# Performance work log

Hardware: AMD Instinct MI355X
Metric: run time of the kernel (lower is better)

The kernel has to match this reference:

```python
import jax, jax.numpy as jnp
import numpy as np


def setup_inputs() -> dict:
    key = jax.random.key(0)
    k_x, k_wxh, k_whh, k_fcw, k_fcb = jax.random.split(key, 5)
    B, T, I, H = 256, 512, 64, 512
    x = jax.random.normal(k_x, (B, T, I), dtype=jnp.float32)
    W_xh = jax.random.normal(k_wxh, (I, H), dtype=jnp.float32) * 0.01
    W_hh = jax.random.normal(k_whh, (H, H), dtype=jnp.float32) * 0.01
    b = jnp.zeros((H,), dtype=jnp.float32)
    # nn.Linear(H, 1): weight (1, H), bias (1); init ~ U(-1/sqrt(H), 1/sqrt(H))
    lim = 1.0 / np.sqrt(H)
    fc_w = jax.random.uniform(k_fcw, (1, H), dtype=jnp.float32, minval=-lim, maxval=lim)
    fc_b = jax.random.uniform(k_fcb, (1,), dtype=jnp.float32, minval=-lim, maxval=lim)
    return {"x": x, "W_xh": W_xh, "W_hh": W_hh, "b": b, "fc_w": fc_w, "fc_b": fc_b}


def reference(x, W_xh, W_hh, b, fc_w, fc_b):
    B, T, I = x.shape
    H = W_hh.shape[0]
    # Precompute input projections for all timesteps in one big matmul: (B,T,H)
    xh = jnp.einsum('bti,ih->bth', x, W_xh) + b
    h0 = jnp.zeros((B, H), dtype=x.dtype)

    def step(h, xh_t):
        h_new = jnp.tanh(xh_t + h @ W_hh)
        return h_new, None

    h_final, _ = jax.lax.scan(step, h0, jnp.swapaxes(xh, 0, 1))  # scan over T
    return h_final @ fc_w.T + fc_b  # (B, 1)
```

## Files before the change

### kernel.cpp

```cpp
#include <hip/hip_runtime.h>


#define BATCH    256
#define TSTEPS   512
#define IDIM     64
#define HDIM     512
#define NTH      512

typedef _Float16 half2_t __attribute__((ext_vector_type(2)));
typedef _Float16 half8_t __attribute__((ext_vector_type(8)));

union H8U {
    half8_t v;
    half2_t p[4];
    uint4   u4;
};

__device__ __forceinline__ float fdot2(half2_t a, half2_t b, float c) {
#if __has_builtin(__builtin_amdgcn_fdot2)
    return __builtin_amdgcn_fdot2(a, b, c, false);
#else
    return c + (float)a[0] * (float)b[0] + (float)a[1] * (float)b[1];
#endif
}

__device__ __forceinline__ float fast_tanh(float x) {
    float e = __builtin_amdgcn_exp2f(x * 2.88539008177792681472f);
    return 1.0f - 2.0f * __builtin_amdgcn_rcpf(e + 1.0f);
}

#define XH_ROWS 16
__global__ __launch_bounds__(NTH, 4)
void xh_gemm(const float* __restrict__ x, const float* __restrict__ Wxh,
             const float* __restrict__ bias, _Float16* __restrict__ xh)
{
    const int j = threadIdx.x;
    const size_t r0 = (size_t)blockIdx.x * XH_ROWS;
    float wcol[IDIM];
#pragma unroll
    for (int i = 0; i < IDIM; ++i) wcol[i] = Wxh[(size_t)i * HDIM + j];
    const float bj = bias[j];
#pragma unroll
    for (int r = 0; r < XH_ROWS; ++r) {
        const float* xr = x + (r0 + r) * IDIM;
        float acc = bj;
#pragma unroll
        for (int i = 0; i < IDIM; ++i) acc += xr[i] * wcol[i];
        xh[(r0 + r) * HDIM + j] = (_Float16)acc;
    }
}

#define S_RP   208
#define S_RC   52
#define S_LC   12
#define S_LSTR 13
#define S_LDSW_BYTES (512 * S_LSTR * 16)
#define S_HBUF_OFF   S_LDSW_BYTES
#define S_HBUF_ELEMS 512
#define S_RED_OFF    (S_HBUF_OFF + 2 * S_HBUF_ELEMS * 2)
#define S_SMEM_BYTES (S_RED_OFF + 64)

__global__ __attribute__((amdgpu_flat_work_group_size(NTH, NTH), amdgpu_waves_per_eu(2, 2)))
void rnn_split(const _Float16* __restrict__ xh,
               const float* __restrict__ Whh,
               const float* __restrict__ fcw,
               const float* __restrict__ fcb,
               float* __restrict__ out)
{
    extern __shared__ char smem[];
    uint4*    ldsW = reinterpret_cast<uint4*>(smem);
    _Float16* hbuf = reinterpret_cast<_Float16*>(smem + S_HBUF_OFF);
    float*    red  = reinterpret_cast<float*>(smem + S_RED_OFF);

    const int j = threadIdx.x;
    const int b = blockIdx.x;

    half2_t wreg[S_RP];
#pragma unroll
    for (int p = 0; p < S_RP; ++p) {
        const int k = 2 * p;
        half2_t w;
        w[0] = (_Float16)Whh[(size_t)k * HDIM + j];
        w[1] = (_Float16)Whh[(size_t)(k + 1) * HDIM + j];
        wreg[p] = w;
    }
#pragma unroll
    for (int cc = 0; cc < S_LC; ++cc) {
        H8U u;
#pragma unroll
        for (int q = 0; q < 4; ++q) {
            const int k0 = 416 + 8 * cc + 2 * q;
            half2_t w;
            w[0] = (_Float16)Whh[(size_t)k0 * HDIM + j];
            w[1] = (_Float16)Whh[(size_t)(k0 + 1) * HDIM + j];
            u.p[q] = w;
        }
        ldsW[j * S_LSTR + cc] = u.u4;
    }

    const float fcwj = fcw[j];
    const _Float16* xhb = xh + (size_t)b * TSTEPS * HDIM;

    hbuf[j] = (_Float16)0.0f;
    __syncthreads();

    float hval = 0.0f;
    for (int t = 0; t < TSTEPS; ++t) {
        const int cur = t & 1;
        const int nxt = cur ^ 1;
        const _Float16* hb = hbuf + cur * S_HBUF_ELEMS;

        const float xv = (float)xhb[(size_t)t * HDIM + j];

        float a0 = 0.0f, a1 = 0.0f, a2 = 0.0f, a3 = 0.0f;
#pragma unroll
        for (int c = 0; c < S_RC; ++c) {
            H8U u;
            u.v = *reinterpret_cast<const half8_t*>(hb + 8 * c);
            a0 = fdot2(u.p[0], wreg[4 * c + 0], a0);
            a1 = fdot2(u.p[1], wreg[4 * c + 1], a1);
            a2 = fdot2(u.p[2], wreg[4 * c + 2], a2);
            a3 = fdot2(u.p[3], wreg[4 * c + 3], a3);
        }
#pragma unroll
        for (int cc = 0; cc < S_LC; ++cc) {
            H8U u, w;
            u.v  = *reinterpret_cast<const half8_t*>(hb + 8 * (S_RC + cc));
            w.u4 = ldsW[j * S_LSTR + cc];
            a0 = fdot2(u.p[0], w.p[0], a0);
            a1 = fdot2(u.p[1], w.p[1], a1);
            a2 = fdot2(u.p[2], w.p[2], a2);
            a3 = fdot2(u.p[3], w.p[3], a3);
        }
        hval = fast_tanh(((a0 + a1) + (a2 + a3)) + xv);

        hbuf[nxt * S_HBUF_ELEMS + j] = (_Float16)hval;
        __syncthreads();
    }

    float partial = hval * fcwj;
#pragma unroll
    for (int off = 32; off >= 1; off >>= 1)
        partial += __shfl_down(partial, off, 64);
    if ((j & 63) == 0) red[j >> 6] = partial;
    __syncthreads();
    if (j == 0) {
        float s = 0.0f;
#pragma unroll
        for (int w = 0; w < 8; ++w) s += red[w];
        out[b] = s + fcb[0];
    }
}

#define F_RP   216
#define F_RC   54
#define F_LC   18
#define F_LSTR 19
#define F_LDSW_BYTES (512 * F_LSTR * 16)
#define F_HBUF_OFF   F_LDSW_BYTES
#define F_HBUF_ELEMS 640
#define F_RED_OFF    (F_HBUF_OFF + 2 * F_HBUF_ELEMS * 2)
#define F_SMEM_BYTES (F_RED_OFF + 64)

__global__ __attribute__((amdgpu_flat_work_group_size(NTH, NTH), amdgpu_waves_per_eu(2, 2)))
void rnn_fused(const float* __restrict__ x, const float* __restrict__ Wxh,
               const float* __restrict__ Whh, const float* __restrict__ bias,
               const float* __restrict__ fcw, const float* __restrict__ fcb,
               float* __restrict__ out)
{
    extern __shared__ char smem[];
    uint4*    ldsW = reinterpret_cast<uint4*>(smem);
    _Float16* hbuf = reinterpret_cast<_Float16*>(smem + F_HBUF_OFF);
    float*    red  = reinterpret_cast<float*>(smem + F_RED_OFF);

    const int j = threadIdx.x;
    const int b = blockIdx.x;

    half2_t wreg[F_RP];
#pragma unroll
    for (int p = 0; p < F_RP; ++p) {
        const int k = 2 * p;
        half2_t w;
        w[0] = (_Float16)Whh[(size_t)k * HDIM + j];
        w[1] = (_Float16)Whh[(size_t)(k + 1) * HDIM + j];
        wreg[p] = w;
    }
#pragma unroll
    for (int cc = 0; cc < F_LC; ++cc) {
        H8U u;
#pragma unroll
        for (int q = 0; q < 4; ++q) {
            const int k0 = 432 + 8 * cc + 2 * q;
            const int k1 = k0 + 1;
            half2_t w;
            w[0] = (_Float16)(k0 < HDIM ? Whh[(size_t)k0 * HDIM + j]
                                        : Wxh[(size_t)(k0 - HDIM) * HDIM + j]);
            w[1] = (_Float16)(k1 < HDIM ? Whh[(size_t)k1 * HDIM + j]
                                        : Wxh[(size_t)(k1 - HDIM) * HDIM + j]);
            u.p[q] = w;
        }
        ldsW[j * F_LSTR + cc] = u.u4;
    }

    const float bj   = bias[j];
    const float fcwj = fcw[j];

    hbuf[j] = (_Float16)0.0f;
    if (j < IDIM) hbuf[HDIM + j] = (_Float16)x[((size_t)b * TSTEPS + 0) * IDIM + j];
    __syncthreads();

    float hval = 0.0f;
    for (int t = 0; t < TSTEPS; ++t) {
        const int cur = t & 1;
        const int nxt = cur ^ 1;
        const _Float16* hb = hbuf + cur * F_HBUF_ELEMS;

        float xv = 0.0f;
        const bool do_x = (j < IDIM) && (t + 1 < TSTEPS);
        if (do_x) xv = x[((size_t)b * TSTEPS + (t + 1)) * IDIM + j];

        float a0 = bj, a1 = 0.0f, a2 = 0.0f, a3 = 0.0f;
#pragma unroll
        for (int c = 0; c < F_RC; ++c) {
            H8U u;
            u.v = *reinterpret_cast<const half8_t*>(hb + 8 * c);
            a0 = fdot2(u.p[0], wreg[4 * c + 0], a0);
            a1 = fdot2(u.p[1], wreg[4 * c + 1], a1);
            a2 = fdot2(u.p[2], wreg[4 * c + 2], a2);
            a3 = fdot2(u.p[3], wreg[4 * c + 3], a3);
        }
#pragma unroll
        for (int cc = 0; cc < F_LC; ++cc) {
            H8U u, w;
            u.v  = *reinterpret_cast<const half8_t*>(hb + 8 * (F_RC + cc));
            w.u4 = ldsW[j * F_LSTR + cc];
            a0 = fdot2(u.p[0], w.p[0], a0);
            a1 = fdot2(u.p[1], w.p[1], a1);
            a2 = fdot2(u.p[2], w.p[2], a2);
            a3 = fdot2(u.p[3], w.p[3], a3);
        }
        hval = fast_tanh((a0 + a1) + (a2 + a3));

        hbuf[nxt * F_HBUF_ELEMS + j] = (_Float16)hval;
        if (do_x) hbuf[nxt * F_HBUF_ELEMS + HDIM + j] = (_Float16)xv;
        __syncthreads();
    }

    float partial = hval * fcwj;
#pragma unroll
    for (int off = 32; off >= 1; off >>= 1)
        partial += __shfl_down(partial, off, 64);
    if ((j & 63) == 0) red[j >> 6] = partial;
    __syncthreads();
    if (j == 0) {
        float s = 0.0f;
#pragma unroll
        for (int w = 0; w < 8; ++w) s += red[w];
        out[b] = s + fcb[0];
    }
}

extern "C" void kernel_launch(void* const* d_in, const int* in_sizes, int n_in,
                              void* d_out, int out_size, void* d_ws, size_t ws_size,
                              hipStream_t stream) {
    const float* x    = (const float*)d_in[0];
    const float* Wxh  = (const float*)d_in[1];
    const float* Whh  = (const float*)d_in[2];
    const float* bias = (const float*)d_in[3];
    const float* fcw  = (const float*)d_in[4];
    const float* fcb  = (const float*)d_in[5];
    float* out = (float*)d_out;

    const size_t xh_bytes = (size_t)BATCH * TSTEPS * HDIM * sizeof(_Float16);
    if (ws_size >= xh_bytes) {
        hipFuncSetAttribute(reinterpret_cast<const void*>(rnn_split),
                            hipFuncAttributeMaxDynamicSharedMemorySize, S_SMEM_BYTES);
        _Float16* xh = (_Float16*)d_ws;
        xh_gemm<<<(BATCH * TSTEPS) / XH_ROWS, NTH, 0, stream>>>(x, Wxh, bias, xh);
        rnn_split<<<BATCH, NTH, S_SMEM_BYTES, stream>>>(xh, Whh, fcw, fcb, out);
    } else {
        hipFuncSetAttribute(reinterpret_cast<const void*>(rnn_fused),
                            hipFuncAttributeMaxDynamicSharedMemorySize, F_SMEM_BYTES);
        rnn_fused<<<BATCH, NTH, F_SMEM_BYTES, stream>>>(x, Wxh, Whh, bias, fcw, fcb, out);
    }
}
```

Baseline: 1.144 ms.

## Split recurrent matvec across thread quads with DPP reduction, 1024 threads per block

Replaces the one-thread-per-hidden-unit recurrence kernel with a 1024-thread version. Each group of four threads covers two hidden units, each thread handles a quarter of the K dimension, and the partial sums are combined with DPP quad reductions. This shortens each thread's serial dot-product chain per timestep and spreads the W_hh fp16 cache over more registers. The h buffer layout is padded to reduce LDS bank conflicts. In exchange it adds cross-lane reduction latency and leaves three of every four lanes idle during the tanh and store.

```diff
diff --git a/kernel.cpp b/kernel.cpp
--- a/kernel.cpp
+++ b/kernel.cpp
@@ -27,6 +27,16 @@
 __device__ __forceinline__ float fast_tanh(float x) {
     float e = __builtin_amdgcn_exp2f(x * 2.88539008177792681472f);
     return 1.0f - 2.0f * __builtin_amdgcn_rcpf(e + 1.0f);
+}
+
+__device__ __forceinline__ float quad_sum(float x) {
+    union { float f; int i; } a, b;
+    a.f = x;
+    b.i = __builtin_amdgcn_update_dpp(0, a.i, 0xB1, 0xF, 0xF, true);
+    a.f += b.f;
+    b.i = __builtin_amdgcn_update_dpp(0, a.i, 0x4E, 0xF, 0xF, true);
+    a.f += b.f;
+    return a.f;
 }
 
 #define XH_ROWS 16
@@ -50,104 +60,139 @@
     }
 }
 
-#define S_RP   208
-#define S_RC   52
-#define S_LC   12
-#define S_LSTR 13
-#define S_LDSW_BYTES (512 * S_LSTR * 16)
-#define S_HBUF_OFF   S_LDSW_BYTES
-#define S_HBUF_ELEMS 512
-#define S_RED_OFF    (S_HBUF_OFF + 2 * S_HBUF_ELEMS * 2)
-#define S_SMEM_BYTES (S_RED_OFF + 64)
-
-__global__ __attribute__((amdgpu_flat_work_group_size(NTH, NTH), amdgpu_waves_per_eu(2, 2)))
-void rnn_split(const _Float16* __restrict__ xh,
-               const float* __restrict__ Whh,
-               const float* __restrict__ fcw,
-               const float* __restrict__ fcb,
-               float* __restrict__ out)
+#define NTH2      1024
+#define Q_CHUNKS  16
+#define Q_AREG    12
+#define Q_BREG    11
+#define Q_LCH     9
+#define Q_LDSW_BYTES (NTH2 * Q_LCH * 16)
+#define Q_HB_OFF     Q_LDSW_BYTES
+#define Q_HB_STRIDE  1152
+#define Q_RED_OFF    (Q_HB_OFF + 2 * Q_HB_STRIDE)
+#define Q_SMEM_BYTES (Q_RED_OFF + 64)
+
+__global__ __attribute__((amdgpu_flat_work_group_size(NTH2, NTH2)))
+void rnn_quad(const _Float16* __restrict__ xh,
+              const float* __restrict__ Whh,
+              const float* __restrict__ fcw,
+              const float* __restrict__ fcb,
+              float* __restrict__ out)
 {
     extern __shared__ char smem[];
-    uint4*    ldsW = reinterpret_cast<uint4*>(smem);
-    _Float16* hbuf = reinterpret_cast<_Float16*>(smem + S_HBUF_OFF);
-    float*    red  = reinterpret_cast<float*>(smem + S_RED_OFF);
-
-    const int j = threadIdx.x;
-    const int b = blockIdx.x;
-
-    half2_t wreg[S_RP];
-#pragma unroll
-    for (int p = 0; p < S_RP; ++p) {
-        const int k = 2 * p;
-        half2_t w;
-        w[0] = (_Float16)Whh[(size_t)k * HDIM + j];
-        w[1] = (_Float16)Whh[(size_t)(k + 1) * HDIM + j];
-        wreg[p] = w;
-    }
-#pragma unroll
-    for (int cc = 0; cc < S_LC; ++cc) {
-        H8U u;
-#pragma unroll
-        for (int q = 0; q < 4; ++q) {
-            const int k0 = 416 + 8 * cc + 2 * q;
-            half2_t w;
-            w[0] = (_Float16)Whh[(size_t)k0 * HDIM + j];
-            w[1] = (_Float16)Whh[(size_t)(k0 + 1) * HDIM + j];
-            u.p[q] = w;
-        }
-        ldsW[j * S_LSTR + cc] = u.u4;
-    }
-
-    const float fcwj = fcw[j];
-    const _Float16* xhb = xh + (size_t)b * TSTEPS * HDIM;
-
-    hbuf[j] = (_Float16)0.0f;
+    uint4* ldsW = reinterpret_cast<uint4*>(smem);
+    float* red  = reinterpret_cast<float*>(smem + Q_RED_OFF);
+
+    const int tid = threadIdx.x;
+    const int q   = tid & 3;
+    const int co  = (tid >> 2) & 15;
+    const int wv  = tid >> 6;
+    const int jA  = wv * 32 + co * 2;
+    const int b   = blockIdx.x;
+
+    half2_t wAr[4 * Q_AREG];
+    half2_t wBr[4 * Q_BREG];
+    uint4*  myW = ldsW + tid * Q_LCH;
+#pragma unroll
+    for (int i = 0; i < Q_CHUNKS; ++i) {
+        H8U a, c;
+#pragma unroll
+        for (int e = 0; e < 4; ++e) {
+            const int k = 128 * q + 8 * i + 2 * e;
+            const float2 r0 = *reinterpret_cast<const float2*>(Whh + (size_t)k * HDIM + jA);
+            const float2 r1 = *reinterpret_cast<const float2*>(Whh + (size_t)(k + 1) * HDIM + jA);
+            half2_t ha; ha[0] = (_Float16)r0.x; ha[1] = (_Float16)r1.x;
+            half2_t hc; hc[0] = (_Float16)r0.y; hc[1] = (_Float16)r1.y;
+            if (i < Q_AREG) wAr[4 * i + e] = ha; else a.p[e] = ha;
+            if (i < Q_BREG) wBr[4 * i + e] = hc; else c.p[e] = hc;
+        }
+        if (i >= Q_AREG) myW[i - Q_AREG]       = a.u4;
+        if (i >= Q_BREG) myW[4 + (i - Q_BREG)] = c.u4;
+    }
+
+    const _Float16* hb0 = reinterpret_cast<const _Float16*>(smem + Q_HB_OFF + 288 * q);
+    const _Float16* hb1 = reinterpret_cast<const _Float16*>(smem + Q_HB_OFF + Q_HB_STRIDE + 288 * q);
+    _Float16* wp0 = reinterpret_cast<_Float16*>(smem + Q_HB_OFF + 2 * jA + 32 * (jA >> 7));
+    _Float16* wp1 = reinterpret_cast<_Float16*>(smem + Q_HB_OFF + Q_HB_STRIDE + 2 * jA + 32 * (jA >> 7));
+
+    const float fcwA = fcw[jA];
+    const float fcwB = fcw[jA + 1];
+    const _Float16* xhp = xh + (size_t)b * TSTEPS * HDIM + jA;
+
+    if (q == 0) {
+        half2_t z; z[0] = (_Float16)0.f; z[1] = (_Float16)0.f;
+        *reinterpret_cast<half2_t*>(wp0) = z;
+    }
     __syncthreads();
 
-    float hval = 0.0f;
+    float hA = 0.f, hB = 0.f;
+#pragma unroll 1
     for (int t = 0; t < TSTEPS; ++t) {
-        const int cur = t & 1;
-        const int nxt = cur ^ 1;
-        const _Float16* hb = hbuf + cur * S_HBUF_ELEMS;
-
-        const float xv = (float)xhb[(size_t)t * HDIM + j];
-
-        float a0 = 0.0f, a1 = 0.0f, a2 = 0.0f, a3 = 0.0f;
-#pragma unroll
-        for (int c = 0; c < S_RC; ++c) {
-            H8U u;
-            u.v = *reinterpret_cast<const half8_t*>(hb + 8 * c);
-            a0 = fdot2(u.p[0], wreg[4 * c + 0], a0);
-            a1 = fdot2(u.p[1], wreg[4 * c + 1], a1);
-            a2 = fdot2(u.p[2], wreg[4 * c + 2], a2);
-            a3 = fdot2(u.p[3], wreg[4 * c + 3], a3);
-        }
-#pragma unroll
-        for (int cc = 0; cc < S_LC; ++cc) {
-            H8U u, w;
-            u.v  = *reinterpret_cast<const half8_t*>(hb + 8 * (S_RC + cc));
-            w.u4 = ldsW[j * S_LSTR + cc];
-            a0 = fdot2(u.p[0], w.p[0], a0);
-            a1 = fdot2(u.p[1], w.p[1], a1);
-            a2 = fdot2(u.p[2], w.p[2], a2);
-            a3 = fdot2(u.p[3], w.p[3], a3);
-        }
-        hval = fast_tanh(((a0 + a1) + (a2 + a3)) + xv);
-
-        hbuf[nxt * S_HBUF_ELEMS + j] = (_Float16)hval;
+        const _Float16* hb = (t & 1) ? hb1 : hb0;
+        const half2_t xv = *reinterpret_cast<const half2_t*>(xhp);
+        xhp += HDIM;
+
+        float a0 = 0.f, a1 = 0.f, c0 = 0.f, c1 = 0.f;
+#pragma unroll
+        for (int i = 0; i < Q_BREG; ++i) {
+            H8U u; u.v = *reinterpret_cast<const half8_t*>(hb + 8 * i);
+            a0 = fdot2(u.p[0], wAr[4*i+0], a0);
+            a1 = fdot2(u.p[1], wAr[4*i+1], a1);
+            a0 = fdot2(u.p[2], wAr[4*i+2], a0);
+            a1 = fdot2(u.p[3], wAr[4*i+3], a1);
+            c0 = fdot2(u.p[0], wBr[4*i+0], c0);
+            c1 = fdot2(u.p[1], wBr[4*i+1], c1);
+            c0 = fdot2(u.p[2], wBr[4*i+2], c0);
+            c1 = fdot2(u.p[3], wBr[4*i+3], c1);
+        }
+        {
+            H8U u; u.v = *reinterpret_cast<const half8_t*>(hb + 8 * 11);
+            H8U wc; wc.u4 = myW[4];
+            a0 = fdot2(u.p[0], wAr[44], a0);
+            a1 = fdot2(u.p[1], wAr[45], a1);
+            a0 = fdot2(u.p[2], wAr[46], a0);
+            a1 = fdot2(u.p[3], wAr[47], a1);
+            c0 = fdot2(u.p[0], wc.p[0], c0);
+            c1 = fdot2(u.p[1], wc.p[1], c1);
+            c0 = fdot2(u.p[2], wc.p[2], c0);
+            c1 = fdot2(u.p[3], wc.p[3], c1);
+        }
+#pragma unroll
+        for (int i = 12; i < 16; ++i) {
+            H8U u; u.v = *reinterpret_cast<const half8_t*>(hb + 8 * i);
+            H8U wa; wa.u4 = myW[i - 12];
+            H8U wc; wc.u4 = myW[i - 7];
+            a0 = fdot2(u.p[0], wa.p[0], a0);
+            a1 = fdot2(u.p[1], wa.p[1], a1);
+            a0 = fdot2(u.p[2], wa.p[2], a0);
+            a1 = fdot2(u.p[3], wa.p[3], a1);
+            c0 = fdot2(u.p[0], wc.p[0], c0);
+            c1 = fdot2(u.p[1], wc.p[1], c1);
+            c0 = fdot2(u.p[2], wc.p[2], c0);
+            c1 = fdot2(u.p[3], wc.p[3], c1);
+        }
+
+        const float sA = quad_sum(a0 + a1);
+        const float sB = quad_sum(c0 + c1);
+
+        if (q == 0) {
+            hA = fast_tanh(sA + (float)xv[0]);
+            hB = fast_tanh(sB + (float)xv[1]);
+            half2_t hw; hw[0] = (_Float16)hA; hw[1] = (_Float16)hB;
+            *reinterpret_cast<half2_t*>((t & 1) ? wp0 : wp1) = hw;
+        }
         __syncthreads();
     }
 
-    float partial = hval * fcwj;
+    float partial = (q == 0) ? (hA * fcwA + hB * fcwB) : 0.f;
 #pragma unroll
     for (int off = 32; off >= 1; off >>= 1)
         partial += __shfl_down(partial, off, 64);
-    if ((j & 63) == 0) red[j >> 6] = partial;
+    if ((tid & 63) == 0) red[tid >> 6] = partial;
     __syncthreads();
-    if (j == 0) {
-        float s = 0.0f;
-#pragma unroll
-        for (int w = 0; w < 8; ++w) s += red[w];
+    if (tid == 0) {
+        float s = 0.f;
+#pragma unroll
+        for (int w = 0; w < 16; ++w) s += red[w];
         out[b] = s + fcb[0];
     }
 }
@@ -189,15 +234,15 @@
     for (int cc = 0; cc < F_LC; ++cc) {
         H8U u;
 #pragma unroll
-        for (int q = 0; q < 4; ++q) {
-            const int k0 = 432 + 8 * cc + 2 * q;
+        for (int qq = 0; qq < 4; ++qq) {
+            const int k0 = 432 + 8 * cc + 2 * qq;
             const int k1 = k0 + 1;
             half2_t w;
             w[0] = (_Float16)(k0 < HDIM ? Whh[(size_t)k0 * HDIM + j]
                                         : Wxh[(size_t)(k0 - HDIM) * HDIM + j]);
             w[1] = (_Float16)(k1 < HDIM ? Whh[(size_t)k1 * HDIM + j]
                                         : Wxh[(size_t)(k1 - HDIM) * HDIM + j]);
-            u.p[q] = w;
+            u.p[qq] = w;
         }
         ldsW[j * F_LSTR + cc] = u.u4;
     }
@@ -273,11 +318,11 @@
 
     const size_t xh_bytes = (size_t)BATCH * TSTEPS * HDIM * sizeof(_Float16);
     if (ws_size >= xh_bytes) {
-        hipFuncSetAttribute(reinterpret_cast<const void*>(rnn_split),
-                            hipFuncAttributeMaxDynamicSharedMemorySize, S_SMEM_BYTES);
+        hipFuncSetAttribute(reinterpret_cast<const void*>(rnn_quad),
+                            hipFuncAttributeMaxDynamicSharedMemorySize, Q_SMEM_BYTES);
         _Float16* xh = (_Float16*)d_ws;
         xh_gemm<<<(BATCH * TSTEPS) / XH_ROWS, NTH, 0, stream>>>(x, Wxh, bias, xh);
-        rnn_split<<<BATCH, NTH, S_SMEM_BYTES, stream>>>(xh, Whh, fcw, fcb, out);
+        rnn_quad<<<BATCH, NTH2, Q_SMEM_BYTES, stream>>>(xh, Whh, fcw, fcb, out);
     } else {
         hipFuncSetAttribute(reinterpret_cast<const void*>(rnn_fused),
                             hipFuncAttributeMaxDynamicSharedMemorySize, F_SMEM_BYTES);
```

Result: slower. 1.425 ms (+24.5%).

## Split RNN recurrence K-dimension across thread quads with DPP reduction

Applied to the files above, without the earlier changes.

The recurrent kernel now gives each thread four output columns over a 128-wide slice of K, instead of one column over the full K. Partial sums are combined across the four threads of a quad with DPP lane swizzles. The h buffer is padded per quarter so that each thread reads only its own slice. This cuts per-thread LDS reads of h by roughly 4x and reuses each loaded h vector across four columns. The cost is the cross-lane reduction and a new, more complex LDS addressing layout.

```diff
diff --git a/kernel.cpp b/kernel.cpp
--- a/kernel.cpp
+++ b/kernel.cpp
@@ -27,6 +27,16 @@
 __device__ __forceinline__ float fast_tanh(float x) {
     float e = __builtin_amdgcn_exp2f(x * 2.88539008177792681472f);
     return 1.0f - 2.0f * __builtin_amdgcn_rcpf(e + 1.0f);
+}
+
+__device__ __forceinline__ float quad_sum(float x) {
+    union { float f; int i; } a, b;
+    a.f = x;
+    b.i = __builtin_amdgcn_update_dpp(0, a.i, 0xB1, 0xF, 0xF, true);
+    a.f += b.f;
+    b.i = __builtin_amdgcn_update_dpp(0, a.i, 0x4E, 0xF, 0xF, true);
+    a.f += b.f;
+    return a.f;
 }
 
 #define XH_ROWS 16
@@ -50,102 +60,138 @@
     }
 }
 
-#define S_RP   208
-#define S_RC   52
-#define S_LC   12
-#define S_LSTR 13
-#define S_LDSW_BYTES (512 * S_LSTR * 16)
-#define S_HBUF_OFF   S_LDSW_BYTES
-#define S_HBUF_ELEMS 512
-#define S_RED_OFF    (S_HBUF_OFF + 2 * S_HBUF_ELEMS * 2)
-#define S_SMEM_BYTES (S_RED_OFF + 64)
+#define K4_RP      48
+#define K4_STR     17
+#define K4_W_BYTES (NTH * K4_STR * 16)
+#define K4_HB_OFF   K4_W_BYTES
+#define K4_HB_STRIDE 1152
+#define K4_RED_OFF  (K4_HB_OFF + 2 * K4_HB_STRIDE)
+#define K4_SMEM_BYTES (K4_RED_OFF + 64)
 
 __global__ __attribute__((amdgpu_flat_work_group_size(NTH, NTH), amdgpu_waves_per_eu(2, 2)))
-void rnn_split(const _Float16* __restrict__ xh,
-               const float* __restrict__ Whh,
-               const float* __restrict__ fcw,
-               const float* __restrict__ fcb,
-               float* __restrict__ out)
+void rnn_k4(const _Float16* __restrict__ xh,
+            const float* __restrict__ Whh,
+            const float* __restrict__ fcw,
+            const float* __restrict__ fcb,
+            float* __restrict__ out)
 {
     extern __shared__ char smem[];
-    uint4*    ldsW = reinterpret_cast<uint4*>(smem);
-    _Float16* hbuf = reinterpret_cast<_Float16*>(smem + S_HBUF_OFF);
-    float*    red  = reinterpret_cast<float*>(smem + S_RED_OFF);
-
-    const int j = threadIdx.x;
-    const int b = blockIdx.x;
-
-    half2_t wreg[S_RP];
-#pragma unroll
-    for (int p = 0; p < S_RP; ++p) {
-        const int k = 2 * p;
+    uint4* ldsW = reinterpret_cast<uint4*>(smem);
+    float* red  = reinterpret_cast<float*>(smem + K4_RED_OFF);
+
+    const int tid   = threadIdx.x;
+    const int q     = tid & 3;
+    const int c     = tid >> 2;
+    const int j0    = 4 * c;
+    const int kbase = 128 * q;
+    const int b     = blockIdx.x;
+
+    half2_t wr0[K4_RP], wr1[K4_RP], wr2[K4_RP], wr3[K4_RP];
+    uint4*  myW = ldsW + tid * K4_STR;
+#pragma unroll
+    for (int p = 0; p < K4_RP; ++p) {
+        const float4 f0 = *reinterpret_cast<const float4*>(Whh + (size_t)(kbase + 2 * p) * HDIM + j0);
+        const float4 f1 = *reinterpret_cast<const float4*>(Whh + (size_t)(kbase + 2 * p + 1) * HDIM + j0);
         half2_t w;
-        w[0] = (_Float16)Whh[(size_t)k * HDIM + j];
-        w[1] = (_Float16)Whh[(size_t)(k + 1) * HDIM + j];
-        wreg[p] = w;
-    }
-#pragma unroll
-    for (int cc = 0; cc < S_LC; ++cc) {
-        H8U u;
-#pragma unroll
-        for (int q = 0; q < 4; ++q) {
-            const int k0 = 416 + 8 * cc + 2 * q;
+        w[0] = (_Float16)f0.x; w[1] = (_Float16)f1.x; wr0[p] = w;
+        w[0] = (_Float16)f0.y; w[1] = (_Float16)f1.y; wr1[p] = w;
+        w[0] = (_Float16)f0.z; w[1] = (_Float16)f1.z; wr2[p] = w;
+        w[0] = (_Float16)f0.w; w[1] = (_Float16)f1.w; wr3[p] = w;
+    }
+#pragma unroll
+    for (int cc = 0; cc < 4; ++cc) {
+        H8U t0, t1, t2, t3;
+#pragma unroll
+        for (int e = 0; e < 4; ++e) {
+            const int k = kbase + 96 + 8 * cc + 2 * e;
+            const float4 f0 = *reinterpret_cast<const float4*>(Whh + (size_t)k * HDIM + j0);
+            const float4 f1 = *reinterpret_cast<const float4*>(Whh + (size_t)(k + 1) * HDIM + j0);
             half2_t w;
-            w[0] = (_Float16)Whh[(size_t)k0 * HDIM + j];
-            w[1] = (_Float16)Whh[(size_t)(k0 + 1) * HDIM + j];
-            u.p[q] = w;
-        }
-        ldsW[j * S_LSTR + cc] = u.u4;
-    }
-
-    const float fcwj = fcw[j];
-    const _Float16* xhb = xh + (size_t)b * TSTEPS * HDIM;
-
-    hbuf[j] = (_Float16)0.0f;
+            w[0] = (_Float16)f0.x; w[1] = (_Float16)f1.x; t0.p[e] = w;
+            w[0] = (_Float16)f0.y; w[1] = (_Float16)f1.y; t1.p[e] = w;
+            w[0] = (_Float16)f0.z; w[1] = (_Float16)f1.z; t2.p[e] = w;
+            w[0] = (_Float16)f0.w; w[1] = (_Float16)f1.w; t3.p[e] = w;
+        }
+        myW[cc]      = t0.u4;
+        myW[4 + cc]  = t1.u4;
+        myW[8 + cc]  = t2.u4;
+        myW[12 + cc] = t3.u4;
+    }
+
+    const char* hb0c = smem + K4_HB_OFF + 288 * q;
+    const char* hb1c = hb0c + K4_HB_STRIDE;
+    const int   jw   = j0 + q;
+    const int   wbyte = 2 * jw + 32 * (jw >> 7);
+    _Float16* wp0 = reinterpret_cast<_Float16*>(smem + K4_HB_OFF + wbyte);
+    _Float16* wp1 = reinterpret_cast<_Float16*>(smem + K4_HB_OFF + K4_HB_STRIDE + wbyte);
+
+    const float fcwj = fcw[jw];
+    const _Float16* xhp = xh + (size_t)b * TSTEPS * HDIM + jw;
+
+    if (tid < 144) {
+        uint4 z; z.x = z.y = z.z = z.w = 0u;
+        reinterpret_cast<uint4*>(smem + K4_HB_OFF)[tid] = z;
+    }
     __syncthreads();
 
-    float hval = 0.0f;
+    float hlast = 0.f;
+#pragma unroll 1
     for (int t = 0; t < TSTEPS; ++t) {
-        const int cur = t & 1;
-        const int nxt = cur ^ 1;
-        const _Float16* hb = hbuf + cur * S_HBUF_ELEMS;
-
-        const float xv = (float)xhb[(size_t)t * HDIM + j];
-
-        float a0 = 0.0f, a1 = 0.0f, a2 = 0.0f, a3 = 0.0f;
-#pragma unroll
-        for (int c = 0; c < S_RC; ++c) {
-            H8U u;
-            u.v = *reinterpret_cast<const half8_t*>(hb + 8 * c);
-            a0 = fdot2(u.p[0], wreg[4 * c + 0], a0);
-            a1 = fdot2(u.p[1], wreg[4 * c + 1], a1);
-            a2 = fdot2(u.p[2], wreg[4 * c + 2], a2);
-            a3 = fdot2(u.p[3], wreg[4 * c + 3], a3);
-        }
-#pragma unroll
-        for (int cc = 0; cc < S_LC; ++cc) {
-            H8U u, w;
-            u.v  = *reinterpret_cast<const half8_t*>(hb + 8 * (S_RC + cc));
-            w.u4 = ldsW[j * S_LSTR + cc];
-            a0 = fdot2(u.p[0], w.p[0], a0);
-            a1 = fdot2(u.p[1], w.p[1], a1);
-            a2 = fdot2(u.p[2], w.p[2], a2);
-            a3 = fdot2(u.p[3], w.p[3], a3);
-        }
-        hval = fast_tanh(((a0 + a1) + (a2 + a3)) + xv);
-
-        hbuf[nxt * S_HBUF_ELEMS + j] = (_Float16)hval;
+        const _Float16* hb = reinterpret_cast<const _Float16*>((t & 1) ? hb1c : hb0c);
+        const float xv = (float)*xhp;
+        xhp += HDIM;
+
+        float a0 = 0.f, b0 = 0.f, a1 = 0.f, b1 = 0.f;
+        float a2 = 0.f, b2 = 0.f, a3 = 0.f, b3 = 0.f;
+#pragma unroll
+        for (int i = 0; i < 12; ++i) {
+            H8U u; u.v = *reinterpret_cast<const half8_t*>(hb + 8 * i);
+            a0 = fdot2(u.p[0], wr0[4*i+0], a0); b0 = fdot2(u.p[1], wr0[4*i+1], b0);
+            a0 = fdot2(u.p[2], wr0[4*i+2], a0); b0 = fdot2(u.p[3], wr0[4*i+3], b0);
+            a1 = fdot2(u.p[0], wr1[4*i+0], a1); b1 = fdot2(u.p[1], wr1[4*i+1], b1);
+            a1 = fdot2(u.p[2], wr1[4*i+2], a1); b1 = fdot2(u.p[3], wr1[4*i+3], b1);
+            a2 = fdot2(u.p[0], wr2[4*i+0], a2); b2 = fdot2(u.p[1], wr2[4*i+1], b2);
+            a2 = fdot2(u.p[2], wr2[4*i+2], a2); b2 = fdot2(u.p[3], wr2[4*i+3], b2);
+            a3 = fdot2(u.p[0], wr3[4*i+0], a3); b3 = fdot2(u.p[1], wr3[4*i+1], b3);
+            a3 = fdot2(u.p[2], wr3[4*i+2], a3); b3 = fdot2(u.p[3], wr3[4*i+3], b3);
+        }
+#pragma unroll
+        for (int cc = 0; cc < 4; ++cc) {
+            H8U u; u.v = *reinterpret_cast<const half8_t*>(hb + 8 * (12 + cc));
+            H8U w0; w0.u4 = myW[cc];
+            H8U w1; w1.u4 = myW[4 + cc];
+            H8U w2; w2.u4 = myW[8 + cc];
+            H8U w3; w3.u4 = myW[12 + cc];
+            a0 = fdot2(u.p[0], w0.p[0], a0); b0 = fdot2(u.p[1], w0.p[1], b0);
+            a0 = fdot2(u.p[2], w0.p[2], a0); b0 = fdot2(u.p[3], w0.p[3], b0);
+            a1 = fdot2(u.p[0], w1.p[0], a1); b1 = fdot2(u.p[1], w1.p[1], b1);
+            a1 = fdot2(u.p[2], w1.p[2], a1); b1 = fdot2(u.p[3], w1.p[3], b1);
+            a2 = fdot2(u.p[0], w2.p[0], a2); b2 = fdot2(u.p[1], w2.p[1], b2);
+            a2 = fdot2(u.p[2], w2.p[2], a2); b2 = fdot2(u.p[3], w2.p[3], b2);
+            a3 = fdot2(u.p[0], w3.p[0], a3); b3 = fdot2(u.p[1], w3.p[1], b3);
+            a3 = fdot2(u.p[2], w3.p[2], a3); b3 = fdot2(u.p[3], w3.p[3], b3);
+        }
+
+        const float s0 = quad_sum(a0 + b0);
+        const float s1 = quad_sum(a1 + b1);
+        const float s2 = quad_sum(a2 + b2);
+        const float s3 = quad_sum(a3 + b3);
+
+        const float sq = (q & 2) ? ((q & 1) ? s3 : s2) : ((q & 1) ? s1 : s0);
+        const float h  = fast_tanh(sq + xv);
+        *((t & 1) ? wp0 : wp1) = (_Float16)h;
+        hlast = h;
         __syncthreads();
     }
 
-    float partial = hval * fcwj;
+    float partial = hlast * fcwj;
 #pragma unroll
     for (int off = 32; off >= 1; off >>= 1)
         partial += __shfl_down(partial, off, 64);
-    if ((j & 63) == 0) red[j >> 6] = partial;
+    if ((tid & 63) == 0) red[tid >> 6] = partial;
     __syncthreads();
-    if (j == 0) {
-        float s = 0.0f;
+    if (tid == 0) {
+        float s = 0.f;
 #pragma unroll
         for (int w = 0; w < 8; ++w) s += red[w];
         out[b] = s + fcb[0];
@@ -189,15 +235,15 @@
     for (int cc = 0; cc < F_LC; ++cc) {
         H8U u;
 #pragma unroll
-        for (int q = 0; q < 4; ++q) {
-            const int k0 = 432 + 8 * cc + 2 * q;
+        for (int qq = 0; qq < 4; ++qq) {
+            const int k0 = 432 + 8 * cc + 2 * qq;
             const int k1 = k0 + 1;
             half2_t w;
             w[0] = (_Float16)(k0 < HDIM ? Whh[(size_t)k0 * HDIM + j]
                                         : Wxh[(size_t)(k0 - HDIM) * HDIM + j]);
             w[1] = (_Float16)(k1 < HDIM ? Whh[(size_t)k1 * HDIM + j]
                                         : Wxh[(size_t)(k1 - HDIM) * HDIM + j]);
-            u.p[q] = w;
+            u.p[qq] = w;
         }
         ldsW[j * F_LSTR + cc] = u.u4;
     }
@@ -273,11 +319,11 @@
 
     const size_t xh_bytes = (size_t)BATCH * TSTEPS * HDIM * sizeof(_Float16);
     if (ws_size >= xh_bytes) {
-        hipFuncSetAttribute(reinterpret_cast<const void*>(rnn_split),
-                            hipFuncAttributeMaxDynamicSharedMemorySize, S_SMEM_BYTES);
+        hipFuncSetAttribute(reinterpret_cast<const void*>(rnn_k4),
+                            hipFuncAttributeMaxDynamicSharedMemorySize, K4_SMEM_BYTES);
         _Float16* xh = (_Float16*)d_ws;
         xh_gemm<<<(BATCH * TSTEPS) / XH_ROWS, NTH, 0, stream>>>(x, Wxh, bias, xh);
-        rnn_split<<<BATCH, NTH, S_SMEM_BYTES, stream>>>(xh, Whh, fcw, fcb, out);
+        rnn_k4<<<BATCH, NTH, K4_SMEM_BYTES, stream>>>(xh, Whh, fcw, fcb, out);
     } else {
         hipFuncSetAttribute(reinterpret_cast<const void*>(rnn_fused),
                             hipFuncAttributeMaxDynamicSharedMemorySize, F_SMEM_BYTES);
```

Measured after the change: 1.243 ms. 8.6% more time.
